# Optimization experiments

Measured on AMD Instinct MI355X. Metric: run time of the kernel, lower is better.

Reference implementation:

```python
import jax, jax.numpy as jnp
import numpy as np
from jax import lax

THR = 0.0
NMS_SIZE = 5
PAD = NMS_SIZE // 2
B, C, H, W = 8, 1, 2048, 2048
# Upper bound on number of surviving peaks: ~1/(2*25) of pixels pass in
# expectation for iid noise; B*H*W//8 is a very safe static cap.
MAX_PEAKS = (B * H * W) // 8


def max_filter(x):
    # torch MaxPool2d(kernel=5, stride=1, padding=2) == max reduce_window
    # with -inf padding, same spatial output shape.
    return lax.reduce_window(
        x, -jnp.inf, lax.max,
        window_dimensions=(1, 1, NMS_SIZE, NMS_SIZE),
        window_strides=(1, 1, 1, 1),
        padding=[(0, 0), (0, 0), (PAD, PAD), (PAD, PAD)],
    )


def setup_inputs() -> dict:
    key = jax.random.key(0)
    scores = jax.random.normal(key, (B, C, H, W), dtype=jnp.float32)
    return {"scores": scores}


def reference(scores):
    # maxima = (scores == maxpool(scores)) & (scores > thr)
    maxima = (scores == max_filter(scores)) & (scores > THR)
    # torch: maxima.nonzero().t()[2:4] -> [2, K] rows = (h, w) coords.
    # jit-safe: fixed-size nonzero, padded with -1 for absent entries.
    idx = jnp.nonzero(maxima, size=MAX_PEAKS, fill_value=-1)
    return jnp.stack([idx[2], idx[3]])  # [2, MAX_PEAKS]
```

## Files before the change

### kernel.cpp

```cpp
#include <hip/hip_runtime.h>
#include <math.h>

#define IMG_W 2048
#define IMG_H 2048
#define BATCH 8
#define MAX_PEAKS ((BATCH * IMG_H * IMG_W) / 8)
#define NWORDS (BATCH * IMG_H * IMG_W / 32)
#define NFILL 2048


#define LOAD3(i)                                                              \
  {                                                                           \
    q##i##L = *(const float4*)pL;                                             \
    q##i##M = *(const float4*)pM;                                             \
    q##i##R = *(const float4*)pR;                                             \
    const size_t stepB =                                                      \
        ((unsigned)(xn - 1) < 2047u) ? (size_t)(IMG_W * 4) : (size_t)0;       \
    pL += stepB;                                                              \
    pM += stepB;                                                              \
    pR += stepB;                                                              \
    ++xn;                                                                     \
  }

#define COMP(i, HS, MS)                                                       \
  {                                                                           \
    const float qlz = fixL ? NEG : q##i##L.z;                                 \
    const float qlw = fixL ? NEG : q##i##L.w;                                 \
    const float qrx = fixR ? NEG : q##i##R.x;                                 \
    const float qry = fixR ? NEG : q##i##R.y;                                 \
    const float4 qm = q##i##M;                                                \
    const float ab = fmaxf(qm.x, qm.y);                                       \
    const float cd = fmaxf(qm.z, qm.w);                                       \
    const float bc = fmaxf(qm.y, qm.z);                                       \
    const float abcd = fmaxf(ab, cd);                                         \
    HS.x = fmaxf(fmaxf(qlz, qlw), fmaxf(ab, qm.z));                           \
    HS.y = fmaxf(qlw, abcd);                                                  \
    HS.z = fmaxf(abcd, qrx);                                                  \
    HS.w = fmaxf(fmaxf(bc, qm.w), fmaxf(qrx, qry));                           \
    MS = qm;                                                                  \
  }

#define OUT(MS, pos)                                                          \
  {                                                                           \
    const float vx = fmaxf(fmaxf(fmaxf(H0.x, H1.x), fmaxf(H2.x, H3.x)), H4.x);\
    const float vy = fmaxf(fmaxf(fmaxf(H0.y, H1.y), fmaxf(H2.y, H3.y)), H4.y);\
    const float vz = fmaxf(fmaxf(fmaxf(H0.z, H1.z), fmaxf(H2.z, H3.z)), H4.z);\
    const float vw = fmaxf(fmaxf(fmaxf(H0.w, H1.w), fmaxf(H2.w, H3.w)), H4.w);\
    unsigned nib = 0;                                                         \
    nib |= (MS.x > 0.0f && MS.x >= vx) ? 1u : 0u;                             \
    nib |= (MS.y > 0.0f && MS.y >= vy) ? 2u : 0u;                             \
    nib |= (MS.z > 0.0f && MS.z >= vz) ? 4u : 0u;                             \
    nib |= (MS.w > 0.0f && MS.w >= vw) ? 8u : 0u;                             \
    bacc |= nib << (4 * (pos));                                               \
  }

#define MERGE(g)                                                              \
  {                                                                           \
    unsigned x = bacc, y;                                                     \
    y = __shfl_xor(x, 4);                                                     \
    x = (lane & 4) ? ((y >> 16) | (x & 0xFFFF0000u))                          \
                   : ((x & 0x0000FFFFu) | (y << 16));                         \
    y = __shfl_xor(x, 2);                                                     \
    x = (lane & 2) ? (((y >> 8) & 0x00FF00FFu) | (x & 0xFF00FF00u))           \
                   : ((x & 0x00FF00FFu) | ((y << 8) & 0xFF00FF00u));          \
    y = __shfl_xor(x, 1);                                                     \
    x = (lane & 1) ? (((y >> 4) & 0x0F0F0F0Fu) | (x & 0xF0F0F0F0u))           \
                   : ((x & 0x0F0F0F0Fu) | ((y << 4) & 0xF0F0F0F0u));          \
    words[wIdx0 + (g) * 512u] = x;                                            \
    cnt += __popc(x);                                                         \
    bacc = 0;                                                                 \
  }

__global__ __launch_bounds__(256, 4) void nms_mask(const float* __restrict__ scores,
                                                   unsigned* __restrict__ words,
                                                   unsigned* __restrict__ bsum2) {
    const int t = threadIdx.x;
    const int lane = t & 63;
    const int wv = t >> 6;
    const int b = blockIdx.x;
    const int L = (b >> 3) + (b & 7) * 256;
    const int img = L >> 8;
    const int rem = L & 255;
    const int strip = rem >> 5;
    const int chunk = rem & 31;
    const int r0 = chunk * 64 + wv * 16;
    const int c0 = strip * 256;
    const int cl = c0 + lane * 4;
    const size_t imgBase = (size_t)img * ((size_t)IMG_H * IMG_W);
    const float NEG = -INFINITY;

    const bool fixL = (lane == 0) && (strip == 0);
    const bool fixR = (lane == 63) && (strip == 7);

    const int rstart = (r0 - 2) < 0 ? 0 : (r0 - 2);
    const char* rowp = (const char*)(scores + imgBase + (size_t)rstart * IMG_W);
    const char* pL = rowp + 4 * (cl - 4) + (fixL ? 16 : 0);
    const char* pM = rowp + 4 * cl;
    const char* pR = rowp + 4 * (cl + 4) - (fixR ? 16 : 0);
    int xn = r0 - 1;

    float4 q0L, q0M, q0R, q1L, q1M, q1R, q2L, q2M, q2R, q3L, q3M, q3R;
    float4 H0, H1, H2, H3, H4;
    float4 m0, m1, m2;

    unsigned cnt = 0, bacc = 0;
    const unsigned wIdx0 =
        (unsigned)(img * IMG_H + r0 + (lane & 7)) * 64u + strip * 8u + (lane >> 3);
    const int cb0 = (img * IMG_H + r0) >> 4;

    LOAD3(0); LOAD3(1); LOAD3(2);
    LOAD3(3); COMP(0, H0, m0);
    LOAD3(0); COMP(1, H1, m1);
    LOAD3(1); COMP(2, H2, m2);
    LOAD3(2); COMP(3, H3, m0);
    LOAD3(3); COMP(0, H4, m1); OUT(m2, 0);
    LOAD3(0); COMP(1, H0, m2); OUT(m0, 1);
    LOAD3(1); COMP(2, H1, m0); OUT(m1, 2);
    LOAD3(2); COMP(3, H2, m1); OUT(m2, 3);
    LOAD3(3); COMP(0, H3, m2); OUT(m0, 4);
    LOAD3(0); COMP(1, H4, m0); OUT(m1, 5);
    LOAD3(1); COMP(2, H0, m1); OUT(m2, 6);
    LOAD3(2); COMP(3, H1, m2); OUT(m0, 7); MERGE(0);
    LOAD3(3); COMP(0, H2, m0); OUT(m1, 0);
    LOAD3(0); COMP(1, H3, m1); OUT(m2, 1);
    LOAD3(1); COMP(2, H4, m2); OUT(m0, 2);
    LOAD3(2); COMP(3, H0, m0); OUT(m1, 3);
    LOAD3(3); COMP(0, H1, m1); OUT(m2, 4);
              COMP(1, H2, m2); OUT(m0, 5);
              COMP(2, H3, m0); OUT(m1, 6);
              COMP(3, H4, m1); OUT(m2, 7); MERGE(1);

    unsigned s = cnt;
    s += __shfl_xor(s, 1);
    s += __shfl_xor(s, 2);
    s += __shfl_xor(s, 4);
    s += __shfl_xor(s, 8);
    s += __shfl_xor(s, 16);
    s += __shfl_xor(s, 32);
    if (lane == 0) bsum2[cb0 * 8 + strip] = s;
}

__global__ __launch_bounds__(256) void nms_scan(const unsigned* __restrict__ bsum2,
                                                unsigned* __restrict__ base) {
    __shared__ unsigned wtot[4];
    const int t = threadIdx.x;
    const int lane = t & 63, wid = t >> 6;
    const uint4* p = (const uint4*)(bsum2 + t * 32);
    unsigned c[4];
#pragma unroll
    for (int i = 0; i < 4; ++i) {
        uint4 a = p[2 * i], bq = p[2 * i + 1];
        c[i] = a.x + a.y + a.z + a.w + bq.x + bq.y + bq.z + bq.w;
    }
    unsigned s0 = c[0], s1 = s0 + c[1], s2 = s1 + c[2], ts = s2 + c[3];
    unsigned sc = ts;
#pragma unroll
    for (int d = 1; d < 64; d <<= 1) {
        unsigned o = __shfl_up(sc, d);
        if (lane >= d) sc += o;
    }
    if (lane == 63) wtot[wid] = sc;
    __syncthreads();
    unsigned wpre = 0;
#pragma unroll
    for (int k = 0; k < 4; ++k) wpre += (k < wid) ? wtot[k] : 0u;
    unsigned excl = wpre + sc - ts;
    ((uint4*)base)[t] = make_uint4(excl, excl + s0, excl + s1, excl + s2);
    if (t == 255) base[1024] = wpre + sc;
}

__global__ __launch_bounds__(256) void nms_compact(const unsigned* __restrict__ words,
                                                   const unsigned* __restrict__ base,
                                                   int* __restrict__ out) {
    const int t = threadIdx.x;
    const int b = blockIdx.x;
    if (b < 1024) {
        __shared__ unsigned wq[4];
        const int lane = t & 63, wid = t >> 6;
        uint4 q = ((const uint4*)(words + b * 1024))[t];
        unsigned wv[4] = {q.x, q.y, q.z, q.w};
        unsigned tsum = __popc(wv[0]) + __popc(wv[1]) + __popc(wv[2]) + __popc(wv[3]);
        unsigned sc = tsum;
#pragma unroll
        for (int d = 1; d < 64; d <<= 1) {
            unsigned o = __shfl_up(sc, d);
            if (lane >= d) sc += o;
        }
        if (lane == 63) wq[wid] = sc;
        __syncthreads();
        unsigned wpre = 0;
#pragma unroll
        for (int k = 0; k < 4; ++k) wpre += (k < wid) ? wq[k] : 0u;
        unsigned off = base[b] + wpre + sc - tsum;

        const unsigned gword0 = (unsigned)b * 1024u + (unsigned)t * 4u;
#pragma unroll
        for (int wi = 0; wi < 4; ++wi) {
            unsigned m = wv[wi];
            unsigned pbase = (gword0 + wi) << 5;
            while (m) {
                int bit = __builtin_ctz(m);
                m &= m - 1;
                unsigned ppix = pbase + (unsigned)bit;
                int hh = (int)((ppix >> 11) & 2047u);
                int ww = (int)(ppix & 2047u);
                if (off < (unsigned)MAX_PEAKS) {
                    out[off] = hh;
                    out[MAX_PEAKS + off] = ww;
                }
                ++off;
            }
        }
    } else {
        unsigned total = base[1024];
        if (total > (unsigned)MAX_PEAKS) total = MAX_PEAKS;
        unsigned tail = (unsigned)MAX_PEAKS - total;
        unsigned fb = (unsigned)(b - 1024);
        unsigned per = (tail + NFILL - 1) / NFILL;
        unsigned s = total + fb * per;
        unsigned e = s + per;
        if (s > (unsigned)MAX_PEAKS) s = MAX_PEAKS;
        if (e > (unsigned)MAX_PEAKS) e = MAX_PEAKS;
        unsigned a = (s + 3u) & ~3u;
        if (a > e) a = e;
        unsigned e4 = e & ~3u;
        if (e4 < a) e4 = a;
        if ((unsigned)t < a - s) {
            out[s + t] = -1;
            out[MAX_PEAKS + s + t] = -1;
        }
        const int4 m4 = make_int4(-1, -1, -1, -1);
        for (unsigned k = a / 4 + t; k < e4 / 4; k += 256) {
            ((int4*)out)[k] = m4;
            ((int4*)(out + MAX_PEAKS))[k] = m4;
        }
        if ((unsigned)t < e - e4) {
            out[e4 + t] = -1;
            out[MAX_PEAKS + e4 + t] = -1;
        }
    }
}

extern "C" void kernel_launch(void* const* d_in, const int* in_sizes, int n_in,
                              void* d_out, int out_size, void* d_ws, size_t ws_size,
                              hipStream_t stream) {
    const float* scores = (const float*)d_in[0];
    int* out = (int*)d_out;
    unsigned* words = (unsigned*)d_ws;
    unsigned* bsum2 = words + NWORDS;
    unsigned* base = bsum2 + 8192;

    nms_mask<<<2048, 256, 0, stream>>>(scores, words, bsum2);
    nms_scan<<<1, 256, 0, stream>>>(bsum2, base);
    nms_compact<<<1024 + NFILL, 256, 0, stream>>>(words, base, out);
}
```

Baseline: 216.6 us.

## Stage score tiles in LDS via direct global-to-LDS loads for NMS mask

The mask kernel now loads a 36-row by 256-column tile, plus halo columns, into shared memory with global_load_lds, then computes the 5x5 max filter from LDS. Before, each thread read overlapping left, middle and right float4 vectors straight from global memory, with the row reads streamed per wave. Each block now covers 32 rows instead of 64, so the grid doubles, and per-wave counts are combined through shared memory before writing the block sums. This removes redundant global loads of neighbour columns, at the cost of LDS traffic, a barrier, and more halo-row reloads because the tiles are smaller.

Result: no change. 218.5 us (+0.9%).

```diff
diff --git a/kernel.cpp b/kernel.cpp
--- a/kernel.cpp
+++ b/kernel.cpp
@@ -8,27 +8,26 @@
 #define NWORDS (BATCH * IMG_H * IMG_W / 32)
 #define NFILL 2048
 
-
-#define LOAD3(i)                                                              \
+#define TROWS 32
+#define SROWS (TROWS + 4)
+#define LROW 66
+
+
+__device__ __forceinline__ void gl_lds16(const float* g, float* l) {
+    __builtin_amdgcn_global_load_lds(
+        (const __attribute__((address_space(1))) unsigned int*)g,
+        (__attribute__((address_space(3))) unsigned int*)l, 16, 0, 0);
+}
+
+#define COMPL(u, HS, MS)                                                      \
   {                                                                           \
-    q##i##L = *(const float4*)pL;                                             \
-    q##i##M = *(const float4*)pM;                                             \
-    q##i##R = *(const float4*)pR;                                             \
-    const size_t stepB =                                                      \
-        ((unsigned)(xn - 1) < 2047u) ? (size_t)(IMG_W * 4) : (size_t)0;       \
-    pL += stepB;                                                              \
-    pM += stepB;                                                              \
-    pR += stepB;                                                              \
-    ++xn;                                                                     \
-  }
-
-#define COMP(i, HS, MS)                                                       \
-  {                                                                           \
-    const float qlz = fixL ? NEG : q##i##L.z;                                 \
-    const float qlw = fixL ? NEG : q##i##L.w;                                 \
-    const float qrx = fixR ? NEG : q##i##R.x;                                 \
-    const float qry = fixR ? NEG : q##i##R.y;                                 \
-    const float4 qm = q##i##M;                                                \
+    const float4 qld = tile[(lb + (u)) * LROW + lane];                        \
+    const float4 qm  = tile[(lb + (u)) * LROW + lane + 1];                    \
+    const float4 qrd = tile[(lb + (u)) * LROW + lane + 2];                    \
+    const float qlz = fixL ? NEG : qld.z;                                     \
+    const float qlw = fixL ? NEG : qld.w;                                     \
+    const float qrx = fixR ? NEG : qrd.x;                                     \
+    const float qry = fixR ? NEG : qrd.y;                                     \
     const float ab = fmaxf(qm.x, qm.y);                                       \
     const float cd = fmaxf(qm.z, qm.w);                                       \
     const float bc = fmaxf(qm.y, qm.z);                                       \
@@ -54,7 +53,7 @@
     bacc |= nib << (4 * (pos));                                               \
   }
 
-#define MERGE(g)                                                              \
+#define MERGE()                                                               \
   {                                                                           \
     unsigned x = bacc, y;                                                     \
     y = __shfl_xor(x, 4);                                                     \
@@ -66,69 +65,73 @@
     y = __shfl_xor(x, 1);                                                     \
     x = (lane & 1) ? (((y >> 4) & 0x0F0F0F0Fu) | (x & 0xF0F0F0F0u))           \
                    : ((x & 0x0F0F0F0Fu) | ((y << 4) & 0xF0F0F0F0u));          \
-    words[wIdx0 + (g) * 512u] = x;                                            \
+    words[wIdx0] = x;                                                         \
     cnt += __popc(x);                                                         \
-    bacc = 0;                                                                 \
   }
 
 __global__ __launch_bounds__(256, 4) void nms_mask(const float* __restrict__ scores,
                                                    unsigned* __restrict__ words,
                                                    unsigned* __restrict__ bsum2) {
+    __shared__ float4 tile[SROWS * LROW];
+    __shared__ unsigned wcnt[4];
     const int t = threadIdx.x;
     const int lane = t & 63;
     const int wv = t >> 6;
     const int b = blockIdx.x;
-    const int L = (b >> 3) + (b & 7) * 256;
-    const int img = L >> 8;
-    const int rem = L & 255;
-    const int strip = rem >> 5;
-    const int chunk = rem & 31;
-    const int r0 = chunk * 64 + wv * 16;
+    const int L = (b >> 3) + (b & 7) * 512;
+    const int img = L >> 9;
+    const int rem = L & 511;
+    const int strip = rem >> 6;
+    const int chunk = rem & 63;
+    const int r0 = chunk * TROWS;
     const int c0 = strip * 256;
-    const int cl = c0 + lane * 4;
     const size_t imgBase = (size_t)img * ((size_t)IMG_H * IMG_W);
+    const float* ibase = scores + imgBase;
     const float NEG = -INFINITY;
 
-    const bool fixL = (lane == 0) && (strip == 0);
-    const bool fixR = (lane == 63) && (strip == 7);
-
-    const int rstart = (r0 - 2) < 0 ? 0 : (r0 - 2);
-    const char* rowp = (const char*)(scores + imgBase + (size_t)rstart * IMG_W);
-    const char* pL = rowp + 4 * (cl - 4) + (fixL ? 16 : 0);
-    const char* pM = rowp + 4 * cl;
-    const char* pR = rowp + 4 * (cl + 4) - (fixR ? 16 : 0);
-    int xn = r0 - 1;
-
-    float4 q0L, q0M, q0R, q1L, q1M, q1R, q2L, q2M, q2R, q3L, q3M, q3R;
-    float4 H0, H1, H2, H3, H4;
-    float4 m0, m1, m2;
-
-    unsigned cnt = 0, bacc = 0;
+    {
+        const float* gl = ibase + c0 + lane * 4;
+#pragma unroll
+        for (int k = 0; k < 9; ++k) {
+            const int rr = wv * 9 + k;
+            int gr = r0 - 2 + rr;
+            gr = gr < 0 ? 0 : (gr > IMG_H - 1 ? IMG_H - 1 : gr);
+            gl_lds16(gl + (size_t)gr * IMG_W, (float*)&tile[rr * LROW + 1]);
+        }
+    }
+    if (wv < 2 && lane < SROWS) {
+        const int rr = lane;
+        int gr = r0 - 2 + rr;
+        gr = gr < 0 ? 0 : (gr > IMG_H - 1 ? IMG_H - 1 : gr);
+        int ec = (wv == 0) ? (c0 - 4) : (c0 + 256);
+        ec = (ec < 0 || ec > IMG_W - 4) ? c0 : ec;
+        tile[rr * LROW + ((wv == 0) ? 0 : 65)] =
+            *(const float4*)(ibase + (size_t)gr * IMG_W + ec);
+    }
+    __syncthreads();
+
+    const bool fixL = (strip == 0) && (lane == 0);
+    const bool fixR = (strip == 7) && (lane == 63);
+    const int lb = wv * 8;
+    float4 H0, H1, H2, H3, H4, m0, m1, m2;
+    unsigned bacc = 0, cnt = 0;
     const unsigned wIdx0 =
-        (unsigned)(img * IMG_H + r0 + (lane & 7)) * 64u + strip * 8u + (lane >> 3);
-    const int cb0 = (img * IMG_H + r0) >> 4;
-
-    LOAD3(0); LOAD3(1); LOAD3(2);
-    LOAD3(3); COMP(0, H0, m0);
-    LOAD3(0); COMP(1, H1, m1);
-    LOAD3(1); COMP(2, H2, m2);
-    LOAD3(2); COMP(3, H3, m0);
-    LOAD3(3); COMP(0, H4, m1); OUT(m2, 0);
-    LOAD3(0); COMP(1, H0, m2); OUT(m0, 1);
-    LOAD3(1); COMP(2, H1, m0); OUT(m1, 2);
-    LOAD3(2); COMP(3, H2, m1); OUT(m2, 3);
-    LOAD3(3); COMP(0, H3, m2); OUT(m0, 4);
-    LOAD3(0); COMP(1, H4, m0); OUT(m1, 5);
-    LOAD3(1); COMP(2, H0, m1); OUT(m2, 6);
-    LOAD3(2); COMP(3, H1, m2); OUT(m0, 7); MERGE(0);
-    LOAD3(3); COMP(0, H2, m0); OUT(m1, 0);
-    LOAD3(0); COMP(1, H3, m1); OUT(m2, 1);
-    LOAD3(1); COMP(2, H4, m2); OUT(m0, 2);
-    LOAD3(2); COMP(3, H0, m0); OUT(m1, 3);
-    LOAD3(3); COMP(0, H1, m1); OUT(m2, 4);
-              COMP(1, H2, m2); OUT(m0, 5);
-              COMP(2, H3, m0); OUT(m1, 6);
-              COMP(3, H4, m1); OUT(m2, 7); MERGE(1);
+        (unsigned)(img * IMG_H + r0 + wv * 8 + (lane & 7)) * 64u +
+        strip * 8u + (lane >> 3);
+
+    COMPL(0, H0, m0);
+    COMPL(1, H1, m1);
+    COMPL(2, H2, m2);
+    COMPL(3, H3, m0);
+    COMPL(4, H4, m1);  OUT(m2, 0);
+    COMPL(5, H0, m2);  OUT(m0, 1);
+    COMPL(6, H1, m0);  OUT(m1, 2);
+    COMPL(7, H2, m1);  OUT(m2, 3);
+    COMPL(8, H3, m2);  OUT(m0, 4);
+    COMPL(9, H4, m0);  OUT(m1, 5);
+    COMPL(10, H0, m1); OUT(m2, 6);
+    COMPL(11, H1, m2); OUT(m0, 7);
+    MERGE();
 
     unsigned s = cnt;
     s += __shfl_xor(s, 1);
@@ -137,7 +140,13 @@
     s += __shfl_xor(s, 8);
     s += __shfl_xor(s, 16);
     s += __shfl_xor(s, 32);
-    if (lane == 0) bsum2[cb0 * 8 + strip] = s;
+    if (lane == 0) wcnt[wv] = s;
+    __syncthreads();
+    if (t == 0) {
+        const int cb0 = (img * IMG_H + r0) >> 4;
+        bsum2[cb0 * 8 + strip] = wcnt[0] + wcnt[1];
+        bsum2[(cb0 + 1) * 8 + strip] = wcnt[2] + wcnt[3];
+    }
 }
 
 __global__ __launch_bounds__(256) void nms_scan(const unsigned* __restrict__ bsum2,
@@ -250,7 +259,7 @@
     unsigned* bsum2 = words + NWORDS;
     unsigned* base = bsum2 + 8192;
 
-    nms_mask<<<2048, 256, 0, stream>>>(scores, words, bsum2);
+    nms_mask<<<4096, 256, 0, stream>>>(scores, words, bsum2);
     nms_scan<<<1, 256, 0, stream>>>(bsum2, base);
     nms_compact<<<1024 + NFILL, 256, 0, stream>>>(words, base, out);
 }
```

## Process 8 columns per lane with full-width row bands in NMS mask kernel

Applied to the files above, without the earlier changes.

Each lane now handles 8 contiguous columns instead of 4, and each block covers a full 2048-wide, 16-row band of one image, so the block count is halved. Neighbour loads shrink from three float4 per row per 4 columns to four float4 per 8 columns, cutting redundant halo traffic. The bit-packing moves from a 3-step shuffle transpose every 8 rows to a byte-packing OR across 4 lanes every row, with 1 in 4 lanes writing each word. The scan is adjusted to the new per-block partial-sum layout, 4 per band. In exchange, register use rises and per-row stores are narrower.

After: 219.9 us. Within noise of the previous version (+1.5%).

```diff
diff --git a/kernel.cpp b/kernel.cpp
--- a/kernel.cpp
+++ b/kernel.cpp
@@ -9,66 +9,64 @@
 #define NFILL 2048
 
 
-#define LOAD3(i)                                                              \
+#define LOADH(Ha, Hb, mA, mB)                                                 \
   {                                                                           \
-    q##i##L = *(const float4*)pL;                                             \
-    q##i##M = *(const float4*)pM;                                             \
-    q##i##R = *(const float4*)pR;                                             \
+    const float4 qL = *(const float4*)(pB + offL);                            \
+    const float4 M0 = *(const float4*)(pB);                                   \
+    const float4 M1 = *(const float4*)(pB + 16);                              \
+    const float4 qR = *(const float4*)(pB + offR);                            \
     const size_t stepB =                                                      \
         ((unsigned)(xn - 1) < 2047u) ? (size_t)(IMG_W * 4) : (size_t)0;       \
-    pL += stepB;                                                              \
-    pM += stepB;                                                              \
-    pR += stepB;                                                              \
+    pB += stepB;                                                              \
     ++xn;                                                                     \
+    const float qlz = fixL ? NEG : qL.z;                                      \
+    const float qlw = fixL ? NEG : qL.w;                                      \
+    const float qrx = fixR ? NEG : qR.x;                                      \
+    const float qry = fixR ? NEG : qR.y;                                      \
+    const float t01 = fmaxf(M0.x, M0.y);                                      \
+    const float t23 = fmaxf(M0.z, M0.w);                                      \
+    const float t45 = fmaxf(M1.x, M1.y);                                      \
+    const float t67 = fmaxf(M1.z, M1.w);                                      \
+    const float t03 = fmaxf(t01, t23);                                        \
+    const float t47 = fmaxf(t45, t67);                                        \
+    Ha.x = fmaxf(fmaxf(qlz, qlw), fmaxf(t01, M0.z));                          \
+    Ha.y = fmaxf(qlw, t03);                                                   \
+    Ha.z = fmaxf(t03, M1.x);                                                  \
+    Ha.w = fmaxf(fmaxf(M0.y, t23), t45);                                      \
+    Hb.x = fmaxf(t23, fmaxf(t45, M1.z));                                      \
+    Hb.y = fmaxf(M0.w, t47);                                                  \
+    Hb.z = fmaxf(t47, qrx);                                                   \
+    Hb.w = fmaxf(fmaxf(M1.y, t67), fmaxf(qrx, qry));                          \
+    mA = M0;                                                                  \
+    mB = M1;                                                                  \
   }
 
-#define COMP(i, HS, MS)                                                       \
+#define OUT(mA, mB, idx)                                                      \
   {                                                                           \
-    const float qlz = fixL ? NEG : q##i##L.z;                                 \
-    const float qlw = fixL ? NEG : q##i##L.w;                                 \
-    const float qrx = fixR ? NEG : q##i##R.x;                                 \
-    const float qry = fixR ? NEG : q##i##R.y;                                 \
-    const float4 qm = q##i##M;                                                \
-    const float ab = fmaxf(qm.x, qm.y);                                       \
-    const float cd = fmaxf(qm.z, qm.w);                                       \
-    const float bc = fmaxf(qm.y, qm.z);                                       \
-    const float abcd = fmaxf(ab, cd);                                         \
-    HS.x = fmaxf(fmaxf(qlz, qlw), fmaxf(ab, qm.z));                           \
-    HS.y = fmaxf(qlw, abcd);                                                  \
-    HS.z = fmaxf(abcd, qrx);                                                  \
-    HS.w = fmaxf(fmaxf(bc, qm.w), fmaxf(qrx, qry));                           \
-    MS = qm;                                                                  \
-  }
-
-#define OUT(MS, pos)                                                          \
-  {                                                                           \
-    const float vx = fmaxf(fmaxf(fmaxf(H0.x, H1.x), fmaxf(H2.x, H3.x)), H4.x);\
-    const float vy = fmaxf(fmaxf(fmaxf(H0.y, H1.y), fmaxf(H2.y, H3.y)), H4.y);\
-    const float vz = fmaxf(fmaxf(fmaxf(H0.z, H1.z), fmaxf(H2.z, H3.z)), H4.z);\
-    const float vw = fmaxf(fmaxf(fmaxf(H0.w, H1.w), fmaxf(H2.w, H3.w)), H4.w);\
-    unsigned nib = 0;                                                         \
-    nib |= (MS.x > 0.0f && MS.x >= vx) ? 1u : 0u;                             \
-    nib |= (MS.y > 0.0f && MS.y >= vy) ? 2u : 0u;                             \
-    nib |= (MS.z > 0.0f && MS.z >= vz) ? 4u : 0u;                             \
-    nib |= (MS.w > 0.0f && MS.w >= vw) ? 8u : 0u;                             \
-    bacc |= nib << (4 * (pos));                                               \
-  }
-
-#define MERGE(g)                                                              \
-  {                                                                           \
-    unsigned x = bacc, y;                                                     \
-    y = __shfl_xor(x, 4);                                                     \
-    x = (lane & 4) ? ((y >> 16) | (x & 0xFFFF0000u))                          \
-                   : ((x & 0x0000FFFFu) | (y << 16));                         \
-    y = __shfl_xor(x, 2);                                                     \
-    x = (lane & 2) ? (((y >> 8) & 0x00FF00FFu) | (x & 0xFF00FF00u))           \
-                   : ((x & 0x00FF00FFu) | ((y << 8) & 0xFF00FF00u));          \
-    y = __shfl_xor(x, 1);                                                     \
-    x = (lane & 1) ? (((y >> 4) & 0x0F0F0F0Fu) | (x & 0xF0F0F0F0u))           \
-                   : ((x & 0x0F0F0F0Fu) | ((y << 4) & 0xF0F0F0F0u));          \
-    words[wIdx0 + (g) * 512u] = x;                                            \
-    cnt += __popc(x);                                                         \
-    bacc = 0;                                                                 \
+    const float vax = fmaxf(fmaxf(fmaxf(Ha0.x, Ha1.x), fmaxf(Ha2.x, Ha3.x)), Ha4.x); \
+    const float vay = fmaxf(fmaxf(fmaxf(Ha0.y, Ha1.y), fmaxf(Ha2.y, Ha3.y)), Ha4.y); \
+    const float vaz = fmaxf(fmaxf(fmaxf(Ha0.z, Ha1.z), fmaxf(Ha2.z, Ha3.z)), Ha4.z); \
+    const float vaw = fmaxf(fmaxf(fmaxf(Ha0.w, Ha1.w), fmaxf(Ha2.w, Ha3.w)), Ha4.w); \
+    const float vbx = fmaxf(fmaxf(fmaxf(Hb0.x, Hb1.x), fmaxf(Hb2.x, Hb3.x)), Hb4.x); \
+    const float vby = fmaxf(fmaxf(fmaxf(Hb0.y, Hb1.y), fmaxf(Hb2.y, Hb3.y)), Hb4.y); \
+    const float vbz = fmaxf(fmaxf(fmaxf(Hb0.z, Hb1.z), fmaxf(Hb2.z, Hb3.z)), Hb4.z); \
+    const float vbw = fmaxf(fmaxf(fmaxf(Hb0.w, Hb1.w), fmaxf(Hb2.w, Hb3.w)), Hb4.w); \
+    unsigned byte = 0;                                                        \
+    byte |= (mA.x > 0.0f && mA.x >= vax) ? 0x01u : 0u;                        \
+    byte |= (mA.y > 0.0f && mA.y >= vay) ? 0x02u : 0u;                        \
+    byte |= (mA.z > 0.0f && mA.z >= vaz) ? 0x04u : 0u;                        \
+    byte |= (mA.w > 0.0f && mA.w >= vaw) ? 0x08u : 0u;                        \
+    byte |= (mB.x > 0.0f && mB.x >= vbx) ? 0x10u : 0u;                        \
+    byte |= (mB.y > 0.0f && mB.y >= vby) ? 0x20u : 0u;                        \
+    byte |= (mB.z > 0.0f && mB.z >= vbz) ? 0x40u : 0u;                        \
+    byte |= (mB.w > 0.0f && mB.w >= vbw) ? 0x80u : 0u;                        \
+    unsigned x = byte << ((lane & 3) * 8);                                    \
+    x |= __shfl_xor(x, 1);                                                    \
+    x |= __shfl_xor(x, 2);                                                    \
+    if ((lane & 3) == 0) {                                                    \
+      words[wIdx0 + (idx) * 64u] = x;                                         \
+      cnt += __popc(x);                                                       \
+    }                                                                         \
   }
 
 __global__ __launch_bounds__(256, 4) void nms_mask(const float* __restrict__ scores,
@@ -78,57 +76,49 @@
     const int lane = t & 63;
     const int wv = t >> 6;
     const int b = blockIdx.x;
-    const int L = (b >> 3) + (b & 7) * 256;
-    const int img = L >> 8;
-    const int rem = L & 255;
-    const int strip = rem >> 5;
-    const int chunk = rem & 31;
-    const int r0 = chunk * 64 + wv * 16;
-    const int c0 = strip * 256;
-    const int cl = c0 + lane * 4;
+    const int img = b & 7;
+    const int band = b >> 3;
+    const int r0 = band * 16;
+    const int cl = wv * 512 + lane * 8;
     const size_t imgBase = (size_t)img * ((size_t)IMG_H * IMG_W);
     const float NEG = -INFINITY;
 
-    const bool fixL = (lane == 0) && (strip == 0);
-    const bool fixR = (lane == 63) && (strip == 7);
+    const bool fixL = (wv == 0) && (lane == 0);
+    const bool fixR = (wv == 3) && (lane == 63);
+    const int offL = fixL ? 0 : -16;
+    const int offR = fixR ? 16 : 32;
 
     const int rstart = (r0 - 2) < 0 ? 0 : (r0 - 2);
-    const char* rowp = (const char*)(scores + imgBase + (size_t)rstart * IMG_W);
-    const char* pL = rowp + 4 * (cl - 4) + (fixL ? 16 : 0);
-    const char* pM = rowp + 4 * cl;
-    const char* pR = rowp + 4 * (cl + 4) - (fixR ? 16 : 0);
+    const char* pB = (const char*)(scores + imgBase + (size_t)rstart * IMG_W + cl);
     int xn = r0 - 1;
 
-    float4 q0L, q0M, q0R, q1L, q1M, q1R, q2L, q2M, q2R, q3L, q3M, q3R;
-    float4 H0, H1, H2, H3, H4;
-    float4 m0, m1, m2;
-
-    unsigned cnt = 0, bacc = 0;
+    float4 Ha0, Ha1, Ha2, Ha3, Ha4, Hb0, Hb1, Hb2, Hb3, Hb4;
+    float4 mA0, mB0, mA1, mB1, mA2, mB2;
+
+    unsigned cnt = 0;
     const unsigned wIdx0 =
-        (unsigned)(img * IMG_H + r0 + (lane & 7)) * 64u + strip * 8u + (lane >> 3);
-    const int cb0 = (img * IMG_H + r0) >> 4;
-
-    LOAD3(0); LOAD3(1); LOAD3(2);
-    LOAD3(3); COMP(0, H0, m0);
-    LOAD3(0); COMP(1, H1, m1);
-    LOAD3(1); COMP(2, H2, m2);
-    LOAD3(2); COMP(3, H3, m0);
-    LOAD3(3); COMP(0, H4, m1); OUT(m2, 0);
-    LOAD3(0); COMP(1, H0, m2); OUT(m0, 1);
-    LOAD3(1); COMP(2, H1, m0); OUT(m1, 2);
-    LOAD3(2); COMP(3, H2, m1); OUT(m2, 3);
-    LOAD3(3); COMP(0, H3, m2); OUT(m0, 4);
-    LOAD3(0); COMP(1, H4, m0); OUT(m1, 5);
-    LOAD3(1); COMP(2, H0, m1); OUT(m2, 6);
-    LOAD3(2); COMP(3, H1, m2); OUT(m0, 7); MERGE(0);
-    LOAD3(3); COMP(0, H2, m0); OUT(m1, 0);
-    LOAD3(0); COMP(1, H3, m1); OUT(m2, 1);
-    LOAD3(1); COMP(2, H4, m2); OUT(m0, 2);
-    LOAD3(2); COMP(3, H0, m0); OUT(m1, 3);
-    LOAD3(3); COMP(0, H1, m1); OUT(m2, 4);
-              COMP(1, H2, m2); OUT(m0, 5);
-              COMP(2, H3, m0); OUT(m1, 6);
-              COMP(3, H4, m1); OUT(m2, 7); MERGE(1);
+        (unsigned)(img * IMG_H + r0) * 64u + (unsigned)wv * 16u + (unsigned)(lane >> 2);
+
+    LOADH(Ha0, Hb0, mA0, mB0);
+    LOADH(Ha1, Hb1, mA1, mB1);
+    LOADH(Ha2, Hb2, mA2, mB2);
+    LOADH(Ha3, Hb3, mA0, mB0);
+    LOADH(Ha4, Hb4, mA1, mB1);  OUT(mA2, mB2, 0);
+    LOADH(Ha0, Hb0, mA2, mB2);  OUT(mA0, mB0, 1);
+    LOADH(Ha1, Hb1, mA0, mB0);  OUT(mA1, mB1, 2);
+    LOADH(Ha2, Hb2, mA1, mB1);  OUT(mA2, mB2, 3);
+    LOADH(Ha3, Hb3, mA2, mB2);  OUT(mA0, mB0, 4);
+    LOADH(Ha4, Hb4, mA0, mB0);  OUT(mA1, mB1, 5);
+    LOADH(Ha0, Hb0, mA1, mB1);  OUT(mA2, mB2, 6);
+    LOADH(Ha1, Hb1, mA2, mB2);  OUT(mA0, mB0, 7);
+    LOADH(Ha2, Hb2, mA0, mB0);  OUT(mA1, mB1, 8);
+    LOADH(Ha3, Hb3, mA1, mB1);  OUT(mA2, mB2, 9);
+    LOADH(Ha4, Hb4, mA2, mB2);  OUT(mA0, mB0, 10);
+    LOADH(Ha0, Hb0, mA0, mB0);  OUT(mA1, mB1, 11);
+    LOADH(Ha1, Hb1, mA1, mB1);  OUT(mA2, mB2, 12);
+    LOADH(Ha2, Hb2, mA2, mB2);  OUT(mA0, mB0, 13);
+    LOADH(Ha3, Hb3, mA0, mB0);  OUT(mA1, mB1, 14);
+    LOADH(Ha4, Hb4, mA1, mB1);  OUT(mA2, mB2, 15);
 
     unsigned s = cnt;
     s += __shfl_xor(s, 1);
@@ -137,7 +127,7 @@
     s += __shfl_xor(s, 8);
     s += __shfl_xor(s, 16);
     s += __shfl_xor(s, 32);
-    if (lane == 0) bsum2[cb0 * 8 + strip] = s;
+    if (lane == 0) bsum2[(img * 128 + band) * 4 + wv] = s;
 }
 
 __global__ __launch_bounds__(256) void nms_scan(const unsigned* __restrict__ bsum2,
@@ -145,12 +135,12 @@
     __shared__ unsigned wtot[4];
     const int t = threadIdx.x;
     const int lane = t & 63, wid = t >> 6;
-    const uint4* p = (const uint4*)(bsum2 + t * 32);
+    const uint4* p = (const uint4*)bsum2 + t * 4;
     unsigned c[4];
 #pragma unroll
     for (int i = 0; i < 4; ++i) {
-        uint4 a = p[2 * i], bq = p[2 * i + 1];
-        c[i] = a.x + a.y + a.z + a.w + bq.x + bq.y + bq.z + bq.w;
+        uint4 a = p[i];
+        c[i] = a.x + a.y + a.z + a.w;
     }
     unsigned s0 = c[0], s1 = s0 + c[1], s2 = s1 + c[2], ts = s2 + c[3];
     unsigned sc = ts;
@@ -248,9 +238,9 @@
     int* out = (int*)d_out;
     unsigned* words = (unsigned*)d_ws;
     unsigned* bsum2 = words + NWORDS;
-    unsigned* base = bsum2 + 8192;
-
-    nms_mask<<<2048, 256, 0, stream>>>(scores, words, bsum2);
+    unsigned* base = bsum2 + 4096;
+
+    nms_mask<<<1024, 256, 0, stream>>>(scores, words, bsum2);
     nms_scan<<<1, 256, 0, stream>>>(bsum2, base);
     nms_compact<<<1024 + NFILL, 256, 0, stream>>>(words, base, out);
 }
```
